# Performance work log

Measured on AMD Instinct MI355X. Metric: run time of the kernel, lower is better.

The kernel has to match this reference:

```python
import jax, jax.numpy as jnp
import numpy as np

# Static configuration (uniform ragged layout: every sequence has the same lengths)
B = 8          # number of sequences
QLEN = 256     # new query tokens per sequence
D = 1024       # embedding_dim
H = 16         # num_attention_heads
HD = D // H    # head dim = 64
FFN = 4096     # ffn_embedding_dim
PAGE = 16      # KV-cache page size
KV_TOTAL = 4096            # total KV length per sequence (prefix + new)
P = KV_TOTAL // PAGE       # pages per sequence = 256
NEW_PAGES = QLEN // PAGE   # pages occupied by the new tokens = 16
NUM_PAGES = B * P          # 2048
PREFIX = KV_TOTAL - QLEN   # cached prefix length per sequence
SCALE = HD ** -0.5
LN_EPS = 1e-5


def layer_norm(x, g, b):
    mu = jnp.mean(x, axis=-1, keepdims=True)
    var = jnp.mean(jnp.square(x - mu), axis=-1, keepdims=True)
    return (x - mu) * jax.lax.rsqrt(var + LN_EPS) * g + b


def setup_inputs() -> dict:
    key = jax.random.key(0)
    ks = jax.random.split(key, 12)
    s = 0.02
    inp = {
        "x": jax.random.normal(ks[0], (B * QLEN, D), jnp.float32),
        "pagetable": jax.random.normal(ks[1], (NUM_PAGES, 2, PAGE, H, HD), jnp.float32) * 0.5,
        "Wq": jax.random.normal(ks[2], (D, D), jnp.float32) * s,
        "bq": jnp.zeros((D,), jnp.float32),
        "Wk": jax.random.normal(ks[3], (D, D), jnp.float32) * s,
        "bk": jnp.zeros((D,), jnp.float32),
        "Wv": jax.random.normal(ks[4], (D, D), jnp.float32) * s,
        "bv": jnp.zeros((D,), jnp.float32),
        "Wo": jax.random.normal(ks[5], (D, D), jnp.float32) * s,
        "bo": jnp.zeros((D,), jnp.float32),
        "ln1_g": jnp.ones((D,), jnp.float32),
        "ln1_b": jnp.zeros((D,), jnp.float32),
        "W1": jax.random.normal(ks[6], (D, FFN), jnp.float32) * s,
        "b1": jnp.zeros((FFN,), jnp.float32),
        "W2": jax.random.normal(ks[7], (FFN, D), jnp.float32) * s,
        "b2": jnp.zeros((D,), jnp.float32),
        "lnf_g": jnp.ones((D,), jnp.float32),
        "lnf_b": jnp.zeros((D,), jnp.float32),
        "qo_indptr": jnp.arange(B + 1, dtype=jnp.int32) * QLEN,
        "paged_kv_indptr": jnp.arange(B + 1, dtype=jnp.int32) * P,
        "paged_kv_indices": jnp.arange(NUM_PAGES, dtype=jnp.int32),
        "paged_kv_last_page_len": jnp.full((B,), PAGE, jnp.int32),
        "layer_idx": 0,
    }
    return inp


def reference(x, pagetable, Wq, bq, Wk, bk, Wv, bv, Wo, bo,
              ln1_g, ln1_b, W1, b1, W2, b2, lnf_g, lnf_b,
              qo_indptr, paged_kv_indptr, paged_kv_indices,
              paged_kv_last_page_len, layer_idx):
    residual = x

    # ---- paged self-attention (post-LN path: layer_norm_first=False) ----
    q = ((x @ Wq + bq) * SCALE).reshape(B, QLEN, H, HD)
    k_new = (x @ Wk + bk).reshape(B, QLEN, H, HD)
    v_new = (x @ Wv + bv).reshape(B, QLEN, H, HD)

    # append new K/V into the last NEW_PAGES pages of each sequence
    page_ids = paged_kv_indices.reshape(B, P)                 # [B, P]
    new_ids = page_ids[:, P - NEW_PAGES:].reshape(-1)         # [B*NEW_PAGES]
    kv_new = jnp.stack([k_new, v_new], axis=2)                # [B, QLEN, 2, H, HD]
    kv_new = kv_new.reshape(B, NEW_PAGES, PAGE, 2, H, HD).transpose(0, 1, 3, 2, 4, 5)
    pt = pagetable.at[new_ids].set(kv_new.reshape(-1, 2, PAGE, H, HD))

    # gather the full paged KV per sequence
    kv = pt[page_ids]                                         # [B, P, 2, PAGE, H, HD]
    K = kv[:, :, 0].reshape(B, KV_TOTAL, H, HD)
    V = kv[:, :, 1].reshape(B, KV_TOTAL, H, HD)

    # streaming-causal mask: query i attends to kv positions <= PREFIX + i
    scores = jnp.einsum("bqhd,bkhd->bhqk", q, K)              # [B, H, QLEN, KV_TOTAL]
    kv_pos = jnp.arange(KV_TOTAL)[None, :]
    q_pos = PREFIX + jnp.arange(QLEN)[:, None]
    scores = jnp.where(kv_pos <= q_pos, scores, jnp.float32(-1e30))
    attn = jax.nn.softmax(scores, axis=-1)
    ctx = jnp.einsum("bhqk,bkhd->bqhd", attn, V).reshape(B * QLEN, D)
    x = ctx @ Wo + bo

    x = residual + x
    x = layer_norm(x, ln1_g, ln1_b)

    # ---- FFN ----
    residual = x
    x = jax.nn.relu(x @ W1 + b1)
    x = x @ W2 + b2
    layer_result = x
    x = residual + x
    x = layer_norm(x, lnf_g, lnf_b)

    return x, layer_result, pt
```

## Files before the change

### kernel.cpp

```cpp
#include <hip/hip_runtime.h>
#include <hip/hip_bf16.h>

typedef unsigned short u16;
typedef __attribute__((ext_vector_type(4))) float f32x4;
typedef __attribute__((ext_vector_type(8))) short short8;

#define MODE_QKV 0
#define MODE_WO  1
#define MODE_F1  2
#define MODE_F2  3

__device__ inline u16 f2bf(float f) {
    __hip_bfloat16 h = __float2bfloat16(f);
    return *(u16*)&h;
}

typedef __attribute__((address_space(3))) unsigned int lds_u32_t;
typedef const __attribute__((address_space(1))) unsigned int glb_u32_t;
__device__ inline void gload16(const u16* g, u16* l) {
    __builtin_amdgcn_global_load_lds((glb_u32_t*)(const void*)g,
                                     (lds_u32_t*)(void*)l, 16, 0, 0);
}

__global__ __launch_bounds__(256) void prep_wx(
    const float* __restrict__ Wq, const float* __restrict__ Wk,
    const float* __restrict__ Wv, const float* __restrict__ x,
    u16* __restrict__ WqkvT, u16* __restrict__ xb) {
    int bid = blockIdx.x;
    int tid = threadIdx.x;
    int tx = tid & 31, ty = tid >> 5;
    if (bid >= 3072) {
        int i = (bid - 3072) * 256 + tid;
        const float4* p = (const float4*)(x + (size_t)i * 8);
        float4 a = p[0], b = p[1];
        u16 t[8] = {f2bf(a.x), f2bf(a.y), f2bf(a.z), f2bf(a.w),
                    f2bf(b.x), f2bf(b.y), f2bf(b.z), f2bf(b.w)};
        *(uint4*)(xb + (size_t)i * 8) = *(const uint4*)t;
        return;
    }
    int m = bid >> 10, r = bid & 1023;
    const float* src = (m == 0) ? Wq : (m == 1) ? Wk : Wv;
    u16* dst = WqkvT + (size_t)m * 1024 * 1024;
    __shared__ float t[32][33];
    int n0 = (r & 31) * 32, k0 = (r >> 5) * 32;
#pragma unroll
    for (int j = 0; j < 32; j += 8)
        t[ty + j][tx] = src[(size_t)(k0 + ty + j) * 1024 + n0 + tx];
    __syncthreads();
#pragma unroll
    for (int j = 0; j < 32; j += 8)
        dst[(size_t)(n0 + ty + j) * 1024 + k0 + tx] = f2bf(t[tx][ty + j]);
}

__global__ __launch_bounds__(256) void ln_wo(const float* __restrict__ p0,
                                             const float* __restrict__ p1,
                                             const float* __restrict__ bo,
                                             const float* __restrict__ resid,
                                             const float* __restrict__ g,
                                             const float* __restrict__ be,
                                             float* __restrict__ outf,
                                             u16* __restrict__ outb) {
    int row = blockIdx.x;
    int tid = threadIdx.x;
    int c = tid * 4;
    size_t o = (size_t)row * 1024 + c;
    f32x4 v = *(const f32x4*)(p0 + o) + *(const f32x4*)(p1 + o)
            + *(const f32x4*)(bo + c) + *(const f32x4*)(resid + o);
    float s = v[0] + v[1] + v[2] + v[3];
#pragma unroll
    for (int m = 1; m < 64; m <<= 1) s += __shfl_xor(s, m, 64);
    __shared__ float red1[4], red2[4];
    int w = tid >> 6;
    if ((tid & 63) == 0) red1[w] = s;
    __syncthreads();
    float mu = (red1[0] + red1[1] + red1[2] + red1[3]) * (1.0f / 1024.0f);
    f32x4 d = v - mu;
    float q = d[0] * d[0] + d[1] * d[1] + d[2] * d[2] + d[3] * d[3];
#pragma unroll
    for (int m = 1; m < 64; m <<= 1) q += __shfl_xor(q, m, 64);
    if ((tid & 63) == 0) red2[w] = q;
    __syncthreads();
    float var = (red2[0] + red2[1] + red2[2] + red2[3]) * (1.0f / 1024.0f);
    float rs = rsqrtf(var + 1e-5f);
    f32x4 gg = *(const f32x4*)(g + c), bb = *(const f32x4*)(be + c);
    f32x4 ov = d * rs * gg + bb;
    *(f32x4*)(outf + o) = ov;
    u16 t[4] = {f2bf(ov[0]), f2bf(ov[1]), f2bf(ov[2]), f2bf(ov[3])};
    *(uint2*)&outb[o] = *(const uint2*)t;
}

__global__ __launch_bounds__(256) void ln_f2(const float* __restrict__ q0,
                                             const float* __restrict__ b2,
                                             const float* __restrict__ xln1f,
                                             const float* __restrict__ g,
                                             const float* __restrict__ be,
                                             float* __restrict__ out_lr,
                                             float* __restrict__ out_x) {
    int row = blockIdx.x;
    int tid = threadIdx.x;
    int c = tid * 4;
    size_t o = (size_t)row * 1024 + c;
    const size_t st = (size_t)2048 * 1024;
    f32x4 v = *(const f32x4*)(q0 + o) + *(const f32x4*)(q0 + st + o)
            + *(const f32x4*)(q0 + 2 * st + o) + *(const f32x4*)(q0 + 3 * st + o)
            + *(const f32x4*)(b2 + c);
    *(f32x4*)(out_lr + o) = v;
    v = v + *(const f32x4*)(xln1f + o);
    float s = v[0] + v[1] + v[2] + v[3];
#pragma unroll
    for (int m = 1; m < 64; m <<= 1) s += __shfl_xor(s, m, 64);
    __shared__ float red1[4], red2[4];
    int w = tid >> 6;
    if ((tid & 63) == 0) red1[w] = s;
    __syncthreads();
    float mu = (red1[0] + red1[1] + red1[2] + red1[3]) * (1.0f / 1024.0f);
    f32x4 d = v - mu;
    float q = d[0] * d[0] + d[1] * d[1] + d[2] * d[2] + d[3] * d[3];
#pragma unroll
    for (int m = 1; m < 64; m <<= 1) q += __shfl_xor(q, m, 64);
    if ((tid & 63) == 0) red2[w] = q;
    __syncthreads();
    float var = (red2[0] + red2[1] + red2[2] + red2[3]) * (1.0f / 1024.0f);
    float rs = rsqrtf(var + 1e-5f);
    f32x4 gg = *(const f32x4*)(g + c), bb = *(const f32x4*)(be + c);
    *(f32x4*)(out_x + o) = d * rs * gg + bb;
}

template <int MODE>
__device__ __forceinline__ void gemm_body(
    u16* As, u16* Bs, int m0, int n0,
    const u16* __restrict__ A, const u16* __restrict__ Bt, int lda, int Kspan, int N,
    const float* __restrict__ bias0, const float* __restrict__ bias1,
    const float* __restrict__ bias2,
    float* __restrict__ o0, u16* __restrict__ ob,
    u16* __restrict__ kbf, u16* __restrict__ vbf, const int* __restrict__ kvidx) {
    int tid = threadIdx.x;
    int l = tid & 63, w = tid >> 6;
    int wr = w >> 1, wc = w & 1;
    int lr = l & 15, lg = l >> 4;
    int lrow8 = l >> 3;
    int scol = ((l & 7) ^ lrow8) << 3;
    f32x4 acc[4][4] = {};
    for (int kb = 0; kb < Kspan; kb += 64) {
#pragma unroll
        for (int p = 0; p < 4; ++p) {
            int chunk = p * 4 + w;
            int r = chunk * 8 + lrow8;
            gload16(&A[(size_t)(m0 + r) * lda + kb + scol], &As[chunk * 512]);
            gload16(&Bt[(size_t)(n0 + r) * lda + kb + scol], &Bs[chunk * 512]);
        }
        __syncthreads();
#pragma unroll
        for (int kk = 0; kk < 2; ++kk) {
            short8 a[4], b[4];
            int c0 = kk * 32 + lg * 8;
#pragma unroll
            for (int mi = 0; mi < 4; mi++) {
                int row = wr * 64 + mi * 16 + lr;
                a[mi] = *(const short8*)&As[row * 64 + (c0 ^ ((row & 7) << 3))];
            }
#pragma unroll
            for (int ni = 0; ni < 4; ni++) {
                int row = wc * 64 + ni * 16 + lr;
                b[ni] = *(const short8*)&Bs[row * 64 + (c0 ^ ((row & 7) << 3))];
            }
#pragma unroll
            for (int mi = 0; mi < 4; mi++)
#pragma unroll
                for (int ni = 0; ni < 4; ni++)
                    acc[mi][ni] = __builtin_amdgcn_mfma_f32_16x16x32_bf16(
                        a[mi], b[ni], acc[mi][ni], 0, 0, 0);
        }
        __syncthreads();
    }
#pragma unroll
    for (int mi = 0; mi < 4; mi++) {
#pragma unroll
        for (int ni = 0; ni < 4; ni++) {
#pragma unroll
            for (int r = 0; r < 4; r++) {
                int row = m0 + wr * 64 + mi * 16 + lg * 4 + r;
                int col = n0 + wc * 64 + ni * 16 + lr;
                float v = acc[mi][ni][r];
                if constexpr (MODE == MODE_QKV) {
                    int sel = col >> 10, c = col & 1023;
                    int b = row >> 8, ii = row & 255;
                    int h = (c >> 6), hd = c & 63;
                    if (sel == 0) {
                        ob[(size_t)row * 1024 + c] = f2bf((v + bias0[c]) * 0.125f);
                    } else if (sel == 1) {
                        float val = v + bias1[c];
                        int page = kvidx[b * 256 + 240 + (ii >> 4)];
                        o0[(size_t)page * 32768 + (size_t)(ii & 15) * 1024 + c] = val;
                        kbf[((size_t)(b * 16 + h) * 4096 + 3840 + ii) * 64 + hd] = f2bf(val);
                    } else {
                        float val = v + bias2[c];
                        int page = kvidx[b * 256 + 240 + (ii >> 4)];
                        o0[(size_t)page * 32768 + 16384 + (size_t)(ii & 15) * 1024 + c] = val;
                        vbf[((size_t)(b * 16 + h) * 64 + hd) * 4096 + 3840 + ii] = f2bf(val);
                    }
                } else if constexpr (MODE == MODE_F1) {
                    float t = v + bias0[col];
                    ob[(size_t)row * N + col] = f2bf(fmaxf(t, 0.0f));
                } else {
                    o0[(size_t)row * N + col] = v;
                }
            }
        }
    }
}

template <int MODE>
__global__ __launch_bounds__(256) void gemm_nt(
    const u16* __restrict__ A, const u16* __restrict__ Bt,
    int lda, int Kspan, int N, int gx, int nper,
    const float* __restrict__ bias0,
    float* __restrict__ o0, u16* __restrict__ ob, size_t osplit) {
    __shared__ __align__(16) u16 smem[128 * 64 * 2];
    int bid = blockIdx.x;
    int split = bid / nper, t = bid % nper;
    gemm_body<MODE>(smem, smem + 128 * 64, (t / gx) * 128, (t % gx) * 128,
                    A + (size_t)split * Kspan, Bt + (size_t)split * Kspan,
                    lda, Kspan, N, bias0, nullptr, nullptr,
                    o0 ? o0 + (size_t)split * osplit : nullptr, ob,
                    nullptr, nullptr, nullptr);
}

__global__ __launch_bounds__(256) void mega_prep(
    const u16* __restrict__ xb, const u16* __restrict__ WqkvT,
    const float* __restrict__ bq, const float* __restrict__ bk,
    const float* __restrict__ bv,
    float* __restrict__ out_pt, u16* __restrict__ qbuf,
    u16* __restrict__ Kbf, u16* __restrict__ Vtbf,
    const float* __restrict__ pgt, const int* __restrict__ kvidx) {
    __shared__ __align__(16) u16 smem[128 * 64 * 2];
    int bid = blockIdx.x;
    int tid = threadIdx.x;
    if (bid < 480) {
        int tile = bid % 60, b = bid / 60;
        int T0 = tile * 64;
        int h = tid >> 4, hd0 = (tid & 15) * 4;
        int pg[4];
#pragma unroll
        for (int pi = 0; pi < 4; ++pi) pg[pi] = kvidx[b * 256 + (T0 >> 4) + pi];
#pragma unroll 4
        for (int it2 = 0; it2 < 64; ++it2) {
            int pi = it2 >> 4, it = it2 & 15;
            const float* src = pgt + (size_t)pg[pi] * 32768;
            float* dst = out_pt + (size_t)pg[pi] * 32768;
            size_t o = (size_t)it * 1024 + tid * 4;
            float4 f = *(const float4*)(src + o);
            *(float4*)(dst + o) = f;
            u16 k4[4] = {f2bf(f.x), f2bf(f.y), f2bf(f.z), f2bf(f.w)};
            size_t kdst = ((size_t)(b * 16 + h) * 4096 + T0 + pi * 16 + it) * 64 + hd0;
            *(uint2*)&Kbf[kdst] = *(const uint2*)k4;
        }
        return;
    }
    if (bid < 960) {
        int vb2 = bid - 480;
        int tile = vb2 % 60, b = vb2 / 60;
        int T0 = tile * 64;
        int pg[4];
#pragma unroll
        for (int pi = 0; pi < 4; ++pi) pg[pi] = kvidx[b * 256 + (T0 >> 4) + pi];
        u16* vt = smem;
        for (int hb2 = 0; hb2 < 8; ++hb2) {
#pragma unroll 4
            for (int it = 0; it < 8; ++it) {
                int ti = it * 8 + (tid >> 5);
                int pi = ti >> 4, tokloc = ti & 15;
                int c4 = (tid & 31) * 4;
                size_t o = (size_t)pg[pi] * 32768 + 16384 + (size_t)tokloc * 1024
                           + hb2 * 128 + c4;
                float4 v = *(const float4*)(pgt + o);
                *(float4*)(out_pt + o) = v;
                u16 v4[4] = {f2bf(v.x), f2bf(v.y), f2bf(v.z), f2bf(v.w)};
                *(uint2*)&vt[ti * 134 + c4] = *(const uint2*)v4;
            }
            __syncthreads();
            int g = tid >> 4, j = tid & 15;
#pragma unroll
            for (int rp = 0; rp < 8; ++rp) {
                int ri = rp * 16 + g;
                int h = hb2 * 2 + (ri >> 6), hd = ri & 63;
                u16 o4[4];
#pragma unroll
                for (int s = 0; s < 4; ++s) o4[s] = vt[(j * 4 + s) * 134 + ri];
                *(uint2*)&Vtbf[((size_t)(b * 16 + h) * 64 + hd) * 4096 + T0 + j * 4] =
                    *(const uint2*)o4;
            }
            __syncthreads();
        }
        return;
    }
    int t = bid - 960;
    gemm_body<MODE_QKV>(smem, smem + 8192, (t / 24) * 128, (t % 24) * 128,
                        xb, WqkvT, 1024, 1024, 3072, bq, bk, bv,
                        out_pt, qbuf, Kbf, Vtbf, kvidx);
}

__global__ __launch_bounds__(512) void attn_kernel(const u16* __restrict__ qb,
                                                   const u16* __restrict__ Kbf,
                                                   const u16* __restrict__ Vtbf,
                                                   float* __restrict__ pOct,
                                                   float* __restrict__ pL,
                                                   const float* __restrict__ Wo,
                                                   const float* __restrict__ W1,
                                                   const float* __restrict__ W2,
                                                   u16* __restrict__ WoT,
                                                   u16* __restrict__ W1T,
                                                   u16* __restrict__ W2T) {
    __shared__ u16 Ks[64 * 64];
    __shared__ u16 Vt[64 * 64];
    __shared__ u16 Ps[8][16 * 64];
    int bid = blockIdx.x;
    int tid = threadIdx.x;
    if (bid >= 1024) {
        int sub = tid >> 8, t2 = tid & 255;
        int wb = (bid - 1024) * 2 + sub;
        const float* src; u16* dst; int K, N, bx, by;
        if (wb < 1024) {
            bx = wb & 31; by = wb >> 5; K = 1024; N = 1024; src = Wo; dst = WoT;
        } else if (wb < 5120) {
            int r = wb - 1024; bx = r & 127; by = r >> 7; K = 1024; N = 4096; src = W1; dst = W1T;
        } else {
            int r = wb - 5120; bx = r & 31; by = r >> 5; K = 4096; N = 1024; src = W2; dst = W2T;
        }
        float* t = sub ? (float*)Vt : (float*)Ks;
        int tx = t2 & 31, ty = t2 >> 5;
        int n0 = bx * 32, k0 = by * 32;
#pragma unroll
        for (int jj = 0; jj < 32; jj += 8)
            t[(ty + jj) * 33 + tx] = src[(size_t)(k0 + ty + jj) * N + n0 + tx];
        __syncthreads();
#pragma unroll
        for (int jj = 0; jj < 32; jj += 8)
            dst[(size_t)(n0 + ty + jj) * K + k0 + tx] = f2bf(t[tx * 33 + ty + jj]);
        return;
    }
    int l = tid & 63, w = tid >> 6;
    int lr = l & 15, lg = l >> 4;
    int x = bid & 7, qt = x >> 2, split = x & 3;
    int h = (bid >> 3) & 15, b = bid >> 7;

    int qrow = qt * 128 + w * 16 + lr;
    const u16* qptr = qb + (size_t)(b * 256 + qrow) * 1024 + h * 64 + lg * 8;
    short8 qf0 = *(const short8*)qptr;
    short8 qf1 = *(const short8*)(qptr + 32);

    const u16* kslab = Kbf + (size_t)(b * 16 + h) * 4096 * 64;
    const u16* vslab = Vtbf + (size_t)(b * 16 + h) * 64 * 4096;

    f32x4 octx[4] = {};
    f32x4 lacc = {};
    short8 ones;
#pragma unroll
    for (int jj = 0; jj < 8; jj++) ones[jj] = (short)0x3F80;

    int qbase = 3840 + qt * 128;
    int ntiles = (qbase + 128) >> 6;
    int tstart = split * 16;
    int tend = min(tstart + 16, ntiles);
    int kt0 = tstart * 64, kt1 = tend * 64;

    int srow = tid >> 3, scol8 = (tid & 7) * 8;
    int sdst = srow * 64 + (scol8 ^ ((srow & 7) << 3));
    const u16* kp = kslab + srow * 64 + scol8;
    const u16* vp = vslab + (size_t)srow * 4096 + scol8;

    uint4 kreg = *(const uint4*)(kp + (size_t)kt0 * 64);
    uint4 vreg = *(const uint4*)(vp + kt0);
    for (int kt = kt0; kt < kt1; kt += 64) {
        *(uint4*)&Ks[sdst] = kreg;
        *(uint4*)&Vt[sdst] = vreg;
        __syncthreads();
        bool hn = (kt + 64) < kt1;
        if (hn) {
            kreg = *(const uint4*)(kp + (size_t)(kt + 64) * 64);
            vreg = *(const uint4*)(vp + kt + 64);
        }
        float P[4][4];
        bool need_mask = (kt + 63 > qbase);
        __builtin_amdgcn_s_setprio(1);
#pragma unroll
        for (int ni = 0; ni < 4; ni++) {
            f32x4 s = {};
            int krow = ni * 16 + lr;
            int swz = (krow & 7) << 3;
            short8 k0 = *(const short8*)&Ks[krow * 64 + ((lg * 8) ^ swz)];
            short8 k1 = *(const short8*)&Ks[krow * 64 + ((32 + lg * 8) ^ swz)];
            s = __builtin_amdgcn_mfma_f32_16x16x32_bf16(qf0, k0, s, 0, 0, 0);
            s = __builtin_amdgcn_mfma_f32_16x16x32_bf16(qf1, k1, s, 0, 0, 0);
            if (need_mask) {
                int col = kt + ni * 16 + lr;
#pragma unroll
                for (int r = 0; r < 4; r++) {
                    int q = qt * 128 + w * 16 + lg * 4 + r;
                    P[ni][r] = (col <= 3840 + q) ? __expf(s[r]) : 0.0f;
                }
            } else {
#pragma unroll
                for (int r = 0; r < 4; r++) P[ni][r] = __expf(s[r]);
            }
        }
        __builtin_amdgcn_s_setprio(0);
#pragma unroll
        for (int ni = 0; ni < 4; ni++)
#pragma unroll
            for (int r = 0; r < 4; r++) {
                int prow = lg * 4 + r;
                Ps[w][prow * 64 + ((ni * 16 + lr) ^ ((prow & 7) << 3))] = f2bf(P[ni][r]);
            }
        __builtin_amdgcn_s_setprio(1);
#pragma unroll
        for (int kk = 0; kk < 2; kk++) {
            int c0 = kk * 32 + lg * 8;
            short8 pf = *(const short8*)&Ps[w][lr * 64 + (c0 ^ ((lr & 7) << 3))];
            lacc = __builtin_amdgcn_mfma_f32_16x16x32_bf16(pf, ones, lacc, 0, 0, 0);
#pragma unroll
            for (int dt = 0; dt < 4; dt++) {
                int vrow = dt * 16 + lr;
                short8 vf = *(const short8*)&Vt[vrow * 64 + (c0 ^ ((vrow & 7) << 3))];
                octx[dt] = __builtin_amdgcn_mfma_f32_16x16x32_bf16(pf, vf, octx[dt], 0, 0, 0);
            }
        }
        __builtin_amdgcn_s_setprio(0);
        __syncthreads();
    }
    size_t obase = (((size_t)(split * 8 + b) * 16 + h) * 256 + qt * 128) * 64;
#pragma unroll
    for (int dt = 0; dt < 4; dt++)
#pragma unroll
        for (int r = 0; r < 4; r++)
            pOct[obase + (size_t)(w * 16 + lg * 4 + r) * 64 + dt * 16 + lr] = octx[dt][r];
    if (lr == 0) {
        size_t lbase = ((size_t)(split * 8 + b) * 16 + h) * 256 + qt * 128;
#pragma unroll
        for (int r = 0; r < 4; r++) pL[lbase + w * 16 + lg * 4 + r] = lacc[r];
    }
}

__global__ __launch_bounds__(256) void attn_combine(const float* __restrict__ pOct,
                                                    const float* __restrict__ pL,
                                                    u16* __restrict__ ctxb) {
    int row = blockIdx.x;
    int b = row >> 8, q = row & 255;
    int tid = threadIdx.x;
    int h = tid >> 4, dq = (tid & 15) * 4;
    size_t stride = (size_t)128 * 256 * 64;
    size_t base = ((size_t)(b * 16 + h) * 256 + q) * 64 + dq;
    size_t lstride = 128 * 256;
    size_t lbase = (size_t)(b * 16 + h) * 256 + q;
    f32x4 s = {};
    float ls = 0.0f;
#pragma unroll
    for (int sp = 0; sp < 4; sp++) {
        f32x4 v = *(const f32x4*)(pOct + sp * stride + base);
        s += v;
        ls += pL[sp * lstride + lbase];
    }
    float inv = 1.0f / ls;
    u16 o[4] = {f2bf(s[0] * inv), f2bf(s[1] * inv), f2bf(s[2] * inv), f2bf(s[3] * inv)};
    *(uint2*)&ctxb[(size_t)row * 1024 + h * 64 + dq] = *(const uint2*)o;
}

extern "C" void kernel_launch(void* const* d_in, const int* in_sizes, int n_in,
                              void* d_out, int out_size, void* d_ws, size_t ws_size,
                              hipStream_t stream) {
    (void)in_sizes; (void)n_in; (void)out_size; (void)ws_size;
    const float* x   = (const float*)d_in[0];
    const float* pgt = (const float*)d_in[1];
    const float* Wq  = (const float*)d_in[2];
    const float* bq  = (const float*)d_in[3];
    const float* Wk  = (const float*)d_in[4];
    const float* bk  = (const float*)d_in[5];
    const float* Wv  = (const float*)d_in[6];
    const float* bv  = (const float*)d_in[7];
    const float* Wo  = (const float*)d_in[8];
    const float* bo  = (const float*)d_in[9];
    const float* ln1g = (const float*)d_in[10];
    const float* ln1b = (const float*)d_in[11];
    const float* W1  = (const float*)d_in[12];
    const float* b1  = (const float*)d_in[13];
    const float* W2  = (const float*)d_in[14];
    const float* b2  = (const float*)d_in[15];
    const float* lnfg = (const float*)d_in[16];
    const float* lnfb = (const float*)d_in[17];
    const int* kvidx = (const int*)d_in[20];

    float* out = (float*)d_out;
    float* out_x  = out;
    float* out_lr = out + 2048 * 1024;
    float* out_pt = out + 2 * 2048 * 1024;

    char* ws = (char*)d_ws;
    size_t off = 0;
    auto alloc = [&](size_t bytes) { void* p = ws + off; off += (bytes + 255) & ~(size_t)255; return p; };
    u16* WqkvT = (u16*)alloc((size_t)3072 * 1024 * 2);
    u16* WoT   = (u16*)alloc((size_t)1024 * 1024 * 2);
    u16* W1T   = (u16*)alloc((size_t)4096 * 1024 * 2);
    u16* W2T   = (u16*)alloc((size_t)1024 * 4096 * 2);
    u16* xb    = (u16*)alloc((size_t)2048 * 1024 * 2);
    u16* qbuf  = (u16*)alloc((size_t)2048 * 1024 * 2);
    u16* ctxb  = (u16*)alloc((size_t)2048 * 1024 * 2);
    char* regB = (char*)alloc((size_t)168 * 1024 * 1024);
    u16* Kbf  = (u16*)regB;
    u16* Vtbf = (u16*)(regB + (size_t)64 * 1024 * 1024);
    float* pOct = (float*)(regB + (size_t)128 * 1024 * 1024);
    float* pL   = (float*)(regB + (size_t)162 * 1024 * 1024);
    float* p0    = (float*)regB;
    float* xln1f = (float*)(regB + (size_t)16 * 1024 * 1024);
    u16*   xln1b = (u16*)(regB + (size_t)24 * 1024 * 1024);
    u16*   hb    = (u16*)(regB + (size_t)32 * 1024 * 1024);
    float* q0    = (float*)(regB + (size_t)128 * 1024 * 1024);

    prep_wx<<<4096, 256, 0, stream>>>(Wq, Wk, Wv, x, WqkvT, xb);
    mega_prep<<<1344, 256, 0, stream>>>(xb, WqkvT, bq, bk, bv,
                                        out_pt, qbuf, Kbf, Vtbf, pgt, kvidx);
    attn_kernel<<<5632, 512, 0, stream>>>(qbuf, Kbf, Vtbf, pOct, pL,
                                          Wo, W1, W2, WoT, W1T, W2T);
    attn_combine<<<2048, 256, 0, stream>>>(pOct, pL, ctxb);
    gemm_nt<MODE_WO><<<256, 256, 0, stream>>>(ctxb, WoT, 1024, 512, 1024, 8, 128,
        nullptr, p0, nullptr, (size_t)2048 * 1024);
    ln_wo<<<2048, 256, 0, stream>>>(p0, p0 + (size_t)2048 * 1024, bo, x,
                                    ln1g, ln1b, xln1f, xln1b);
    gemm_nt<MODE_F1><<<512, 256, 0, stream>>>(xln1b, W1T, 1024, 1024, 4096, 32, 512,
        b1, nullptr, hb, 0);
    gemm_nt<MODE_F2><<<512, 256, 0, stream>>>(hb, W2T, 4096, 1024, 1024, 8, 128,
        nullptr, q0, nullptr, (size_t)2048 * 1024);
    ln_f2<<<2048, 256, 0, stream>>>(q0, b2, xln1f, lnfg, lnfb, out_lr, out_x);
}
```

Before: 330.7 us.

## Reorder mega_prep blocks, split pagetable copy out, store partial attention in bf16

mega_prep now runs the QKV GEMM blocks first, then a separate set of blocks that copy the prefix pagetable pages straight to the output. The K and V conversion blocks no longer write the fp32 copy themselves. The grid grows to hold the new copy blocks. Attention partial outputs are stored as bf16 instead of fp32, which halves split-KV traffic into attn_combine but adds rounding error to the partial sums.

```diff
diff --git a/kernel.cpp b/kernel.cpp
--- a/kernel.cpp
+++ b/kernel.cpp
@@ -13,6 +13,9 @@
 __device__ inline u16 f2bf(float f) {
     __hip_bfloat16 h = __float2bfloat16(f);
     return *(u16*)&h;
+}
+__device__ inline float bf2f(u16 u) {
+    union { unsigned int i; float f; } x; x.i = ((unsigned int)u) << 16; return x.f;
 }
 
 typedef __attribute__((address_space(3))) unsigned int lds_u32_t;
@@ -236,8 +239,29 @@
     __shared__ __align__(16) u16 smem[128 * 64 * 2];
     int bid = blockIdx.x;
     int tid = threadIdx.x;
-    if (bid < 480) {
-        int tile = bid % 60, b = bid / 60;
+    if (bid < 384) {
+        gemm_body<MODE_QKV>(smem, smem + 8192, (bid / 24) * 128, (bid % 24) * 128,
+                            xb, WqkvT, 1024, 1024, 3072, bq, bk, bv,
+                            out_pt, qbuf, Kbf, Vtbf, kvidx);
+        return;
+    }
+    if (bid < 1344) {
+        int idx = (bid - 384) * 2;
+#pragma unroll
+        for (int pp = 0; pp < 2; ++pp) {
+            int p = idx + pp;
+            int b = p / 240, slot = p % 240;
+            int page = kvidx[b * 256 + slot];
+            const float4* s = (const float4*)(pgt + (size_t)page * 32768);
+            float4* d = (float4*)(out_pt + (size_t)page * 32768);
+#pragma unroll 8
+            for (int it = 0; it < 32; ++it) d[it * 256 + tid] = s[it * 256 + tid];
+        }
+        return;
+    }
+    if (bid < 1824) {
+        int idx = bid - 1344;
+        int tile = idx % 60, b = idx / 60;
         int T0 = tile * 64;
         int h = tid >> 4, hd0 = (tid & 15) * 4;
         int pg[4];
@@ -247,63 +271,53 @@
         for (int it2 = 0; it2 < 64; ++it2) {
             int pi = it2 >> 4, it = it2 & 15;
             const float* src = pgt + (size_t)pg[pi] * 32768;
-            float* dst = out_pt + (size_t)pg[pi] * 32768;
             size_t o = (size_t)it * 1024 + tid * 4;
             float4 f = *(const float4*)(src + o);
-            *(float4*)(dst + o) = f;
             u16 k4[4] = {f2bf(f.x), f2bf(f.y), f2bf(f.z), f2bf(f.w)};
             size_t kdst = ((size_t)(b * 16 + h) * 4096 + T0 + pi * 16 + it) * 64 + hd0;
             *(uint2*)&Kbf[kdst] = *(const uint2*)k4;
         }
         return;
     }
-    if (bid < 960) {
-        int vb2 = bid - 480;
-        int tile = vb2 % 60, b = vb2 / 60;
-        int T0 = tile * 64;
-        int pg[4];
-#pragma unroll
-        for (int pi = 0; pi < 4; ++pi) pg[pi] = kvidx[b * 256 + (T0 >> 4) + pi];
-        u16* vt = smem;
-        for (int hb2 = 0; hb2 < 8; ++hb2) {
+    int vb2 = bid - 1824;
+    int tile = vb2 % 60, b = vb2 / 60;
+    int T0 = tile * 64;
+    int pg[4];
+#pragma unroll
+    for (int pi = 0; pi < 4; ++pi) pg[pi] = kvidx[b * 256 + (T0 >> 4) + pi];
+    u16* vt = smem;
+    for (int hb2 = 0; hb2 < 8; ++hb2) {
 #pragma unroll 4
-            for (int it = 0; it < 8; ++it) {
-                int ti = it * 8 + (tid >> 5);
-                int pi = ti >> 4, tokloc = ti & 15;
-                int c4 = (tid & 31) * 4;
-                size_t o = (size_t)pg[pi] * 32768 + 16384 + (size_t)tokloc * 1024
-                           + hb2 * 128 + c4;
-                float4 v = *(const float4*)(pgt + o);
-                *(float4*)(out_pt + o) = v;
-                u16 v4[4] = {f2bf(v.x), f2bf(v.y), f2bf(v.z), f2bf(v.w)};
-                *(uint2*)&vt[ti * 134 + c4] = *(const uint2*)v4;
-            }
-            __syncthreads();
-            int g = tid >> 4, j = tid & 15;
-#pragma unroll
-            for (int rp = 0; rp < 8; ++rp) {
-                int ri = rp * 16 + g;
-                int h = hb2 * 2 + (ri >> 6), hd = ri & 63;
-                u16 o4[4];
-#pragma unroll
-                for (int s = 0; s < 4; ++s) o4[s] = vt[(j * 4 + s) * 134 + ri];
-                *(uint2*)&Vtbf[((size_t)(b * 16 + h) * 64 + hd) * 4096 + T0 + j * 4] =
-                    *(const uint2*)o4;
-            }
-            __syncthreads();
-        }
-        return;
-    }
-    int t = bid - 960;
-    gemm_body<MODE_QKV>(smem, smem + 8192, (t / 24) * 128, (t % 24) * 128,
-                        xb, WqkvT, 1024, 1024, 3072, bq, bk, bv,
-                        out_pt, qbuf, Kbf, Vtbf, kvidx);
+        for (int it = 0; it < 8; ++it) {
+            int ti = it * 8 + (tid >> 5);
+            int pi = ti >> 4, tokloc = ti & 15;
+            int c4 = (tid & 31) * 4;
+            size_t o = (size_t)pg[pi] * 32768 + 16384 + (size_t)tokloc * 1024
+                       + hb2 * 128 + c4;
+            float4 v = *(const float4*)(pgt + o);
+            u16 v4[4] = {f2bf(v.x), f2bf(v.y), f2bf(v.z), f2bf(v.w)};
+            *(uint2*)&vt[ti * 134 + c4] = *(const uint2*)v4;
+        }
+        __syncthreads();
+        int g = tid >> 4, j = tid & 15;
+#pragma unroll
+        for (int rp = 0; rp < 8; ++rp) {
+            int ri = rp * 16 + g;
+            int h = hb2 * 2 + (ri >> 6), hd = ri & 63;
+            u16 o4[4];
+#pragma unroll
+            for (int s = 0; s < 4; ++s) o4[s] = vt[(j * 4 + s) * 134 + ri];
+            *(uint2*)&Vtbf[((size_t)(b * 16 + h) * 64 + hd) * 4096 + T0 + j * 4] =
+                *(const uint2*)o4;
+        }
+        __syncthreads();
+    }
 }
 
 __global__ __launch_bounds__(512) void attn_kernel(const u16* __restrict__ qb,
                                                    const u16* __restrict__ Kbf,
                                                    const u16* __restrict__ Vtbf,
-                                                   float* __restrict__ pOct,
+                                                   u16* __restrict__ pOct,
                                                    float* __restrict__ pL,
                                                    const float* __restrict__ Wo,
                                                    const float* __restrict__ W1,
@@ -433,7 +447,8 @@
     for (int dt = 0; dt < 4; dt++)
 #pragma unroll
         for (int r = 0; r < 4; r++)
-            pOct[obase + (size_t)(w * 16 + lg * 4 + r) * 64 + dt * 16 + lr] = octx[dt][r];
+            pOct[obase + (size_t)(w * 16 + lg * 4 + r) * 64 + dt * 16 + lr] =
+                f2bf(octx[dt][r]);
     if (lr == 0) {
         size_t lbase = ((size_t)(split * 8 + b) * 16 + h) * 256 + qt * 128;
 #pragma unroll
@@ -441,7 +456,7 @@
     }
 }
 
-__global__ __launch_bounds__(256) void attn_combine(const float* __restrict__ pOct,
+__global__ __launch_bounds__(256) void attn_combine(const u16* __restrict__ pOct,
                                                     const float* __restrict__ pL,
                                                     u16* __restrict__ ctxb) {
     int row = blockIdx.x;
@@ -456,8 +471,10 @@
     float ls = 0.0f;
 #pragma unroll
     for (int sp = 0; sp < 4; sp++) {
-        f32x4 v = *(const f32x4*)(pOct + sp * stride + base);
-        s += v;
+        u16 a[4];
+        *(uint2*)a = *(const uint2*)&pOct[sp * stride + base];
+#pragma unroll
+        for (int j = 0; j < 4; j++) s[j] += bf2f(a[j]);
         ls += pL[sp * lstride + lbase];
     }
     float inv = 1.0f / ls;
@@ -507,7 +524,7 @@
     char* regB = (char*)alloc((size_t)168 * 1024 * 1024);
     u16* Kbf  = (u16*)regB;
     u16* Vtbf = (u16*)(regB + (size_t)64 * 1024 * 1024);
-    float* pOct = (float*)(regB + (size_t)128 * 1024 * 1024);
+    u16*   pOct = (u16*)(regB + (size_t)128 * 1024 * 1024);
     float* pL   = (float*)(regB + (size_t)162 * 1024 * 1024);
     float* p0    = (float*)regB;
     float* xln1f = (float*)(regB + (size_t)16 * 1024 * 1024);
@@ -516,7 +533,7 @@
     float* q0    = (float*)(regB + (size_t)128 * 1024 * 1024);
 
     prep_wx<<<4096, 256, 0, stream>>>(Wq, Wk, Wv, x, WqkvT, xb);
-    mega_prep<<<1344, 256, 0, stream>>>(xb, WqkvT, bq, bk, bv,
+    mega_prep<<<2304, 256, 0, stream>>>(xb, WqkvT, bq, bk, bv,
                                         out_pt, qbuf, Kbf, Vtbf, pgt, kvidx);
     attn_kernel<<<5632, 512, 0, stream>>>(qbuf, Kbf, Vtbf, pOct, pL,
                                           Wo, W1, W2, WoT, W1T, W2T);
```

Result: slower. 353.2 us (+6.8%).
